# Kernel tuning notes

Measured on AMD Instinct MI355X. Metric: run time of the kernel, lower is better.

The kernel has to match this reference:

```python
import jax, jax.numpy as jnp
import numpy as np

SQRT_2_OVER_PI = 0.7978845608028654

def gelu_new(x):
    # HF 'gelu_new': 0.5*x*(1+tanh(sqrt(2/pi)*(x+0.044715*x^3)))
    return 0.5 * x * (1.0 + jnp.tanh(SQRT_2_OVER_PI * (x + 0.044715 * x * x * x)))

def phm_linear(x, phm_rule, W_left, W_right, bias, n):
    # x: [..., n*p]; phm_rule: [n, n, n]; W_left: [n, p, r]; W_right: [n, r, q]
    # H = sum_i kron(phm_rule[i], W_i), W_i = W_left[i] @ W_right[i]; y = x @ H + b
    p = x.shape[-1] // n
    W = jnp.einsum('ipk,ikq->ipq', W_left, W_right)          # [n, p, q]
    xr = x.reshape(x.shape[:-1] + (n, p))                    # [..., n, p]
    # kron(A,B)[a*p+r, c*q+s] = A[a,c]*B[r,s]
    y = jnp.einsum('...ap,iac,ipq->...cq', xr, phm_rule, W)  # [..., n, q]
    y = y.reshape(x.shape[:-1] + (n * W.shape[-1],))
    return y + bias

def setup_inputs() -> dict:
    key = jax.random.key(0)
    ks = jax.random.split(key, 7)
    B, S, D, d, n = 8, 4096, 768, 192, 4
    x = jax.random.normal(ks[0], (B, S, D), dtype=jnp.float32)
    phm_rule_d = jax.random.normal(ks[1], (n, n, n), dtype=jnp.float32) * 0.01
    W_left_d = jax.random.normal(ks[2], (n, D // n, 1), dtype=jnp.float32) * 0.05
    W_right_d = jax.random.normal(ks[3], (n, 1, d // n), dtype=jnp.float32) * 0.05
    bias_d = jnp.zeros((d,), dtype=jnp.float32)
    phm_rule_u = jax.random.normal(ks[4], (n, n, n), dtype=jnp.float32) * 0.01
    W_left_u = jax.random.normal(ks[5], (n, d // n, 1), dtype=jnp.float32) * 0.05
    W_right_u = jax.random.normal(ks[6], (n, 1, D // n), dtype=jnp.float32) * 0.05
    bias_u = jnp.zeros((D,), dtype=jnp.float32)
    return {"x": x, "phm_rule_d": phm_rule_d, "W_left_d": W_left_d, "W_right_d": W_right_d,
            "bias_d": bias_d, "phm_rule_u": phm_rule_u, "W_left_u": W_left_u,
            "W_right_u": W_right_u, "bias_u": bias_u}

def reference(x, phm_rule_d, W_left_d, W_right_d, bias_d, phm_rule_u, W_left_u, W_right_u, bias_u):
    n = phm_rule_d.shape[0]
    z = phm_linear(x, phm_rule_d, W_left_d, W_right_d, bias_d, n)
    z = gelu_new(z)
    return phm_linear(z, phm_rule_u, W_left_u, W_right_u, bias_u, n)
```

## Files before the change

kernel.cpp:

```cpp
#include <hip/hip_runtime.h>
#include <math.h>


#define SQ2PI 0.79788456080286535588f

typedef float vfloat4 __attribute__((ext_vector_type(4)));
typedef unsigned int vuint2 __attribute__((ext_vector_type(2)));

template<int CTRL>
__device__ __forceinline__ float ror_add(float v) {
    int s = __builtin_amdgcn_update_dpp(0, __float_as_int(v), CTRL, 0xF, 0xF, true);
    return v + __int_as_float(s);
}
__device__ __forceinline__ float reduce16(float v) {
    v = ror_add<0x121>(v);
    v = ror_add<0x122>(v);
    v = ror_add<0x124>(v);
    v = ror_add<0x128>(v);
    return v;
}

__device__ __forceinline__ void swap16(float& d, float& s) {
    vuint2 t = __builtin_amdgcn_permlane16_swap(__float_as_uint(d), __float_as_uint(s), false, false);
    d = __uint_as_float(t.x);  s = __uint_as_float(t.y);
}
__device__ __forceinline__ void swap32(float& d, float& s) {
    vuint2 t = __builtin_amdgcn_permlane32_swap(__float_as_uint(d), __float_as_uint(s), false, false);
    d = __uint_as_float(t.x);  s = __uint_as_float(t.y);
}
__device__ __forceinline__ void bcast4(float h, float& b0, float& b1, float& b2, float& b3) {
    float y1 = h, y2 = h;
    swap16(y1, y2);
    b0 = y1; b2 = y1; swap32(b0, b2);
    b1 = y2; b3 = y2; swap32(b1, b3);
}

__device__ __forceinline__ void nt_store4(float* p, const float4& v) {
    vfloat4 nv;
    nv.x = v.x; nv.y = v.y; nv.z = v.z; nv.w = v.w;
    __builtin_nontemporal_store(nv, (vfloat4*)p);
}

struct Slot { float4 a0[3]; float4 a1[3]; };

__global__ __launch_bounds__(256)
void phm_fused(const float* __restrict__ x,
               const float* __restrict__ rule_d,
               const float* __restrict__ Wl_d,
               const float* __restrict__ Wr_d,
               const float* __restrict__ bias_d,
               const float* __restrict__ rule_u,
               const float* __restrict__ Wl_u,
               const float* __restrict__ Wr_u,
               const float* __restrict__ bias_u,
               float* __restrict__ out,
               int n_tokens)
{
    __shared__ __attribute__((aligned(16))) float sLd[768];
    __shared__ __attribute__((aligned(16))) float sRu[768];
    __shared__ __attribute__((aligned(16))) float sBu[768];
    __shared__ __attribute__((aligned(16))) float sLu[192];
    __shared__ float sBd[192];
    __shared__ float sRd[192];
    __shared__ float sRuleD[64];
    __shared__ float sRuleU[64];

    const int tid = threadIdx.x;
    for (int i = tid; i < 768; i += 256) sLd[i] = Wl_d[i];
    for (int i = tid; i < 768; i += 256) sRu[i] = Wr_u[i];
    for (int i = tid; i < 768; i += 256) sBu[i] = bias_u[i];
    if (tid < 192) {
        sLu[tid] = Wl_u[tid];
        sBd[tid] = bias_d[tid];
        sRd[tid] = Wr_d[tid];
    }
    if (tid < 64)       sRuleD[tid]     = rule_d[tid];
    else if (tid < 128) sRuleU[tid-64]  = rule_u[tid-64];

    const int lane = tid & 63;
    const int wave = tid >> 6;
    const int a    = lane >> 4;
    const int r    = lane & 15;
    const int off  = 192*a + 4*r;

    __syncthreads();

    const int wid     = blockIdx.x * 4 + wave;
    const int n_waves = gridDim.x * 4;
    const int n_pairs = n_tokens >> 1;

    auto issue = [&](Slot& S, int p) {
        const float* xp = x + (size_t)p * 1536 + off;
        #pragma unroll
        for (int u = 0; u < 3; ++u) {
            S.a0[u] = *(const float4*)(xp + 64*u);
            S.a1[u] = *(const float4*)(xp + 768 + 64*u);
        }
    };

    auto compute_store = [&](Slot& S, int p) {
        float s0[4] = {0,0,0,0}, s1[4] = {0,0,0,0};
        #pragma unroll
        for (int u = 0; u < 3; ++u) {
            const float4 xa = S.a0[u];
            const float4 xb = S.a1[u];
            #pragma unroll
            for (int i = 0; i < 4; ++i) {
                const float4 lv = *(const float4*)&sLd[i*192 + 4*r + 64*u];
                s0[i] = fmaf(xa.x, lv.x, s0[i]);  s1[i] = fmaf(xb.x, lv.x, s1[i]);
                s0[i] = fmaf(xa.y, lv.y, s0[i]);  s1[i] = fmaf(xb.y, lv.y, s1[i]);
                s0[i] = fmaf(xa.z, lv.z, s0[i]);  s1[i] = fmaf(xb.z, lv.z, s1[i]);
                s0[i] = fmaf(xa.w, lv.w, s0[i]);  s1[i] = fmaf(xb.w, lv.w, s1[i]);
            }
        }

        float tD0[4], tD1[4];
        #pragma unroll
        for (int i = 0; i < 4; ++i) {
            const float rk0 = sRuleD[i*16 +  0 + a];
            const float rk1 = sRuleD[i*16 +  4 + a];
            const float rk2 = sRuleD[i*16 +  8 + a];
            const float rk3 = sRuleD[i*16 + 12 + a];
            float b0, b1, b2, b3;
            bcast4(reduce16(s0[i]), b0, b1, b2, b3);
            tD0[i] = fmaf(b0, rk0, fmaf(b1, rk1, fmaf(b2, rk2, b3 * rk3)));
            bcast4(reduce16(s1[i]), b0, b1, b2, b3);
            tD1[i] = fmaf(b0, rk0, fmaf(b1, rk1, fmaf(b2, rk2, b3 * rk3)));
        }

        float g0[3], g1[3];
        #pragma unroll
        for (int w = 0; w < 3; ++w) {
            float z0 = sBd[a*48 + 3*r + w], z1 = z0;
            #pragma unroll
            for (int i = 0; i < 4; ++i) {
                const float rd = sRd[i*48 + 3*r + w];
                z0 = fmaf(tD0[i], rd, z0);
                z1 = fmaf(tD1[i], rd, z1);
            }
            const float i0 = SQ2PI * fmaf(0.044715f*z0, z0*z0, z0);
            const float i1 = SQ2PI * fmaf(0.044715f*z1, z1*z1, z1);
            const float e0 = __expf(2.0f*i0);
            const float e1 = __expf(2.0f*i1);
            g0[w] = 0.5f*z0*(1.0f + (1.0f - 2.0f/(e0 + 1.0f)));
            g1[w] = 0.5f*z1*(1.0f + (1.0f - 2.0f/(e1 + 1.0f)));
        }

        float tU0[4], tU1[4];
        #pragma unroll
        for (int i = 0; i < 4; ++i) {
            const float l0 = sLu[i*48 + 3*r + 0];
            const float l1 = sLu[i*48 + 3*r + 1];
            const float l2 = sLu[i*48 + 3*r + 2];
            const float rk0 = sRuleU[i*16 +  0 + a];
            const float rk1 = sRuleU[i*16 +  4 + a];
            const float rk2 = sRuleU[i*16 +  8 + a];
            const float rk3 = sRuleU[i*16 + 12 + a];
            float a0 = g0[0]*l0 + g0[1]*l1 + g0[2]*l2;
            float a1 = g1[0]*l0 + g1[1]*l1 + g1[2]*l2;
            float b0, b1, b2, b3;
            bcast4(reduce16(a0), b0, b1, b2, b3);
            tU0[i] = fmaf(b0, rk0, fmaf(b1, rk1, fmaf(b2, rk2, b3 * rk3)));
            bcast4(reduce16(a1), b0, b1, b2, b3);
            tU1[i] = fmaf(b0, rk0, fmaf(b1, rk1, fmaf(b2, rk2, b3 * rk3)));
        }

        float* op = out + (size_t)p * 1536 + off;
        #pragma unroll
        for (int u = 0; u < 3; ++u) {
            const float4 bv = *(const float4*)&sBu[off + 64*u];
            float4 ov0 = bv, ov1 = bv;
            #pragma unroll
            for (int i = 0; i < 4; ++i) {
                const float4 ru = *(const float4*)&sRu[i*192 + 4*r + 64*u];
                ov0.x = fmaf(tU0[i], ru.x, ov0.x);  ov1.x = fmaf(tU1[i], ru.x, ov1.x);
                ov0.y = fmaf(tU0[i], ru.y, ov0.y);  ov1.y = fmaf(tU1[i], ru.y, ov1.y);
                ov0.z = fmaf(tU0[i], ru.z, ov0.z);  ov1.z = fmaf(tU1[i], ru.z, ov1.z);
                ov0.w = fmaf(tU0[i], ru.w, ov0.w);  ov1.w = fmaf(tU1[i], ru.w, ov1.w);
            }
            nt_store4(op + 64*u,       ov0);
            nt_store4(op + 768 + 64*u, ov1);
        }
    };

    int cnt = 0;
    for (int p = wid; p < n_pairs; p += n_waves) ++cnt;

    Slot S0, S1, S2;
    if (cnt > 0)  issue(S0, wid);
    if (cnt > 1)  issue(S1, wid + n_waves);
    if (cnt > 2)  issue(S2, wid + 2*n_waves);

    int pr = wid;
    for (int k = 0; k + 2 < cnt; k += 3) {
        compute_store(S0, pr);
        if (k + 3 < cnt) issue(S0, pr + 3*n_waves);
        compute_store(S1, pr + n_waves);
        if (k + 4 < cnt) issue(S1, pr + 4*n_waves);
        compute_store(S2, pr + 2*n_waves);
        if (k + 5 < cnt) issue(S2, pr + 5*n_waves);
        pr += 3*n_waves;
    }
    const int rem = cnt % 3;
    const int done = cnt - rem;
    if (rem > 0) compute_store((done % 3 == 0) ? S0 : (done % 3 == 1) ? S1 : S2, pr);
    if (rem > 1) compute_store((done % 3 == 0) ? S1 : (done % 3 == 1) ? S2 : S0, pr + n_waves);
}

extern "C" void kernel_launch(void* const* d_in, const int* in_sizes, int n_in,
                              void* d_out, int out_size, void* d_ws, size_t ws_size,
                              hipStream_t stream) {
    const float* x      = (const float*)d_in[0];
    const float* rule_d = (const float*)d_in[1];
    const float* Wl_d   = (const float*)d_in[2];
    const float* Wr_d   = (const float*)d_in[3];
    const float* bias_d = (const float*)d_in[4];
    const float* rule_u = (const float*)d_in[5];
    const float* Wl_u   = (const float*)d_in[6];
    const float* Wr_u   = (const float*)d_in[7];
    const float* bias_u = (const float*)d_in[8];
    float* out          = (float*)d_out;

    const int n_tokens = in_sizes[0] / 768;

    phm_fused<<<dim3(1024), dim3(256), 0, stream>>>(
        x, rule_d, Wl_d, Wr_d, bias_d, rule_u, Wl_u, Wr_u, bias_u, out, n_tokens);
}
```

Before: 203.9 us.

## Process one token per wave iteration with double-buffered prefetch and larger grid

Replaces the two-tokens-per-iteration, triple-buffered slot pipeline with a simpler loop that handles one token per wave and prefetches the next token's inputs into registers. The grid grows from a fixed 1024 blocks to one block per 16 tokens, so each wave handles about four tokens instead of many. The aim is lower register pressure and higher occupancy, plus more waves in flight to hide memory latency. In exchange it gives up the per-pair instruction amortisation and the deeper per-wave prefetch, and pays more block startup and shared-memory weight loading.

```diff
diff --git a/kernel.cpp b/kernel.cpp
--- a/kernel.cpp
+++ b/kernel.cpp
@@ -40,8 +40,6 @@
     nv.x = v.x; nv.y = v.y; nv.z = v.z; nv.w = v.w;
     __builtin_nontemporal_store(nv, (vfloat4*)p);
 }
-
-struct Slot { float4 a0[3]; float4 a1[3]; };
 
 __global__ __launch_bounds__(256)
 void phm_fused(const float* __restrict__ x,
@@ -87,34 +85,37 @@
 
     const int wid     = blockIdx.x * 4 + wave;
     const int n_waves = gridDim.x * 4;
-    const int n_pairs = n_tokens >> 1;
 
-    auto issue = [&](Slot& S, int p) {
-        const float* xp = x + (size_t)p * 1536 + off;
+    float4 A0, A1, A2;
+    if (wid < n_tokens) {
+        const float* xp = x + (size_t)wid * 768 + off;
+        A0 = *(const float4*)(xp);
+        A1 = *(const float4*)(xp + 64);
+        A2 = *(const float4*)(xp + 128);
+    }
+
+    for (int t = wid; t < n_tokens; t += n_waves) {
+        const int tn = t + n_waves;
+        const float* np = x + (size_t)(tn < n_tokens ? tn : t) * 768 + off;
+        float4 B0 = *(const float4*)(np);
+        float4 B1 = *(const float4*)(np + 64);
+        float4 B2 = *(const float4*)(np + 128);
+
+        float s[4] = {0,0,0,0};
         #pragma unroll
-        for (int u = 0; u < 3; ++u) {
-            S.a0[u] = *(const float4*)(xp + 64*u);
-            S.a1[u] = *(const float4*)(xp + 768 + 64*u);
-        }
-    };
-
-    auto compute_store = [&](Slot& S, int p) {
-        float s0[4] = {0,0,0,0}, s1[4] = {0,0,0,0};
-        #pragma unroll
-        for (int u = 0; u < 3; ++u) {
-            const float4 xa = S.a0[u];
-            const float4 xb = S.a1[u];
-            #pragma unroll
-            for (int i = 0; i < 4; ++i) {
-                const float4 lv = *(const float4*)&sLd[i*192 + 4*r + 64*u];
-                s0[i] = fmaf(xa.x, lv.x, s0[i]);  s1[i] = fmaf(xb.x, lv.x, s1[i]);
-                s0[i] = fmaf(xa.y, lv.y, s0[i]);  s1[i] = fmaf(xb.y, lv.y, s1[i]);
-                s0[i] = fmaf(xa.z, lv.z, s0[i]);  s1[i] = fmaf(xb.z, lv.z, s1[i]);
-                s0[i] = fmaf(xa.w, lv.w, s0[i]);  s1[i] = fmaf(xb.w, lv.w, s1[i]);
-            }
+        for (int i = 0; i < 4; ++i) {
+            const float4 l0 = *(const float4*)&sLd[i*192 + 4*r];
+            const float4 l1 = *(const float4*)&sLd[i*192 + 4*r + 64];
+            const float4 l2 = *(const float4*)&sLd[i*192 + 4*r + 128];
+            s[i] = fmaf(A0.x, l0.x, s[i]);  s[i] = fmaf(A0.y, l0.y, s[i]);
+            s[i] = fmaf(A0.z, l0.z, s[i]);  s[i] = fmaf(A0.w, l0.w, s[i]);
+            s[i] = fmaf(A1.x, l1.x, s[i]);  s[i] = fmaf(A1.y, l1.y, s[i]);
+            s[i] = fmaf(A1.z, l1.z, s[i]);  s[i] = fmaf(A1.w, l1.w, s[i]);
+            s[i] = fmaf(A2.x, l2.x, s[i]);  s[i] = fmaf(A2.y, l2.y, s[i]);
+            s[i] = fmaf(A2.z, l2.z, s[i]);  s[i] = fmaf(A2.w, l2.w, s[i]);
         }
 
-        float tD0[4], tD1[4];
+        float tD[4];
         #pragma unroll
         for (int i = 0; i < 4; ++i) {
             const float rk0 = sRuleD[i*16 +  0 + a];
@@ -122,31 +123,23 @@
             const float rk2 = sRuleD[i*16 +  8 + a];
             const float rk3 = sRuleD[i*16 + 12 + a];
             float b0, b1, b2, b3;
-            bcast4(reduce16(s0[i]), b0, b1, b2, b3);
-            tD0[i] = fmaf(b0, rk0, fmaf(b1, rk1, fmaf(b2, rk2, b3 * rk3)));
-            bcast4(reduce16(s1[i]), b0, b1, b2, b3);
-            tD1[i] = fmaf(b0, rk0, fmaf(b1, rk1, fmaf(b2, rk2, b3 * rk3)));
+            bcast4(reduce16(s[i]), b0, b1, b2, b3);
+            tD[i] = fmaf(b0, rk0, fmaf(b1, rk1, fmaf(b2, rk2, b3 * rk3)));
         }
 
-        float g0[3], g1[3];
+        float g[3];
         #pragma unroll
         for (int w = 0; w < 3; ++w) {
-            float z0 = sBd[a*48 + 3*r + w], z1 = z0;
+            float z = sBd[a*48 + 3*r + w];
             #pragma unroll
-            for (int i = 0; i < 4; ++i) {
-                const float rd = sRd[i*48 + 3*r + w];
-                z0 = fmaf(tD0[i], rd, z0);
-                z1 = fmaf(tD1[i], rd, z1);
-            }
-            const float i0 = SQ2PI * fmaf(0.044715f*z0, z0*z0, z0);
-            const float i1 = SQ2PI * fmaf(0.044715f*z1, z1*z1, z1);
-            const float e0 = __expf(2.0f*i0);
-            const float e1 = __expf(2.0f*i1);
-            g0[w] = 0.5f*z0*(1.0f + (1.0f - 2.0f/(e0 + 1.0f)));
-            g1[w] = 0.5f*z1*(1.0f + (1.0f - 2.0f/(e1 + 1.0f)));
+            for (int i = 0; i < 4; ++i)
+                z = fmaf(tD[i], sRd[i*48 + 3*r + w], z);
+            const float iv = SQ2PI * fmaf(0.044715f*z, z*z, z);
+            const float e  = __expf(2.0f*iv);
+            g[w] = 0.5f*z*(1.0f + (1.0f - 2.0f/(e + 1.0f)));
         }
 
-        float tU0[4], tU1[4];
+        float tU[4];
         #pragma unroll
         for (int i = 0; i < 4; ++i) {
             const float l0 = sLu[i*48 + 3*r + 0];
@@ -156,55 +149,29 @@
             const float rk1 = sRuleU[i*16 +  4 + a];
             const float rk2 = sRuleU[i*16 +  8 + a];
             const float rk3 = sRuleU[i*16 + 12 + a];
-            float a0 = g0[0]*l0 + g0[1]*l1 + g0[2]*l2;
-            float a1 = g1[0]*l0 + g1[1]*l1 + g1[2]*l2;
+            float a0 = g[0]*l0 + g[1]*l1 + g[2]*l2;
             float b0, b1, b2, b3;
             bcast4(reduce16(a0), b0, b1, b2, b3);
-            tU0[i] = fmaf(b0, rk0, fmaf(b1, rk1, fmaf(b2, rk2, b3 * rk3)));
-            bcast4(reduce16(a1), b0, b1, b2, b3);
-            tU1[i] = fmaf(b0, rk0, fmaf(b1, rk1, fmaf(b2, rk2, b3 * rk3)));
+            tU[i] = fmaf(b0, rk0, fmaf(b1, rk1, fmaf(b2, rk2, b3 * rk3)));
         }
 
-        float* op = out + (size_t)p * 1536 + off;
+        float* op = out + (size_t)t * 768 + off;
         #pragma unroll
         for (int u = 0; u < 3; ++u) {
-            const float4 bv = *(const float4*)&sBu[off + 64*u];
-            float4 ov0 = bv, ov1 = bv;
+            float4 ov = *(const float4*)&sBu[off + 64*u];
             #pragma unroll
             for (int i = 0; i < 4; ++i) {
                 const float4 ru = *(const float4*)&sRu[i*192 + 4*r + 64*u];
-                ov0.x = fmaf(tU0[i], ru.x, ov0.x);  ov1.x = fmaf(tU1[i], ru.x, ov1.x);
-                ov0.y = fmaf(tU0[i], ru.y, ov0.y);  ov1.y = fmaf(tU1[i], ru.y, ov1.y);
-                ov0.z = fmaf(tU0[i], ru.z, ov0.z);  ov1.z = fmaf(tU1[i], ru.z, ov1.z);
-                ov0.w = fmaf(tU0[i], ru.w, ov0.w);  ov1.w = fmaf(tU1[i], ru.w, ov1.w);
+                ov.x = fmaf(tU[i], ru.x, ov.x);
+                ov.y = fmaf(tU[i], ru.y, ov.y);
+                ov.z = fmaf(tU[i], ru.z, ov.z);
+                ov.w = fmaf(tU[i], ru.w, ov.w);
             }
-            nt_store4(op + 64*u,       ov0);
-            nt_store4(op + 768 + 64*u, ov1);
+            nt_store4(op + 64*u, ov);
         }
-    };
 
-    int cnt = 0;
-    for (int p = wid; p < n_pairs; p += n_waves) ++cnt;
-
-    Slot S0, S1, S2;
-    if (cnt > 0)  issue(S0, wid);
-    if (cnt > 1)  issue(S1, wid + n_waves);
-    if (cnt > 2)  issue(S2, wid + 2*n_waves);
-
-    int pr = wid;
-    for (int k = 0; k + 2 < cnt; k += 3) {
-        compute_store(S0, pr);
-        if (k + 3 < cnt) issue(S0, pr + 3*n_waves);
-        compute_store(S1, pr + n_waves);
-        if (k + 4 < cnt) issue(S1, pr + 4*n_waves);
-        compute_store(S2, pr + 2*n_waves);
-        if (k + 5 < cnt) issue(S2, pr + 5*n_waves);
-        pr += 3*n_waves;
+        A0 = B0; A1 = B1; A2 = B2;
     }
-    const int rem = cnt % 3;
-    const int done = cnt - rem;
-    if (rem > 0) compute_store((done % 3 == 0) ? S0 : (done % 3 == 1) ? S1 : S2, pr);
-    if (rem > 1) compute_store((done % 3 == 0) ? S1 : (done % 3 == 1) ? S2 : S0, pr + n_waves);
 }
 
 extern "C" void kernel_launch(void* const* d_in, const int* in_sizes, int n_in,
@@ -223,6 +190,7 @@
 
     const int n_tokens = in_sizes[0] / 768;
 
-    phm_fused<<<dim3(1024), dim3(256), 0, stream>>>(
+    const int blocks = (n_tokens + 15) / 16;
+    phm_fused<<<dim3(blocks), dim3(256), 0, stream>>>(
         x, rule_d, Wl_d, Wr_d, bias_d, rule_u, Wl_u, Wr_u, bias_u, out, n_tokens);
 }
```

Result: faster. 196.6 us (-3.6%).
